# Performance work log

Hardware: AMD Instinct MI355X
Metric: run time of the kernel (lower is better)

Reference implementation:

```python
import jax, jax.numpy as jnp
import numpy as np
import math

COV_WEIGHT = 1.0
BANDWIDTH_FACTOR = 1.06
SQRT_2PI = math.sqrt(2.0 * math.pi)
EPS_LOG = 1e-8
H_MIN = 1e-4


def setup_inputs() -> dict:
    key = jax.random.key(0)
    activity = jax.random.normal(key, (2048, 64), dtype=jnp.float32)
    return {"activity": activity}


def reference(activity):
    B, R = activity.shape
    # Silverman bandwidth per receptor (torch .std uses ddof=1)
    std = jnp.std(activity, axis=0, ddof=1)                     # (R,)
    h = jnp.maximum(BANDWIDTH_FACTOR * std * (B ** (-0.2)), H_MIN)  # (R,)

    # Pairwise Gaussian KDE: query == samples == activity
    u = (activity[:, None, :] - activity[None, :, :]) / h       # (B_q, B_s, R)
    kernel_values = jnp.exp(-0.5 * u * u) / SQRT_2PI             # (B_q, B_s, R)
    density = kernel_values.sum(axis=1) / (B * h)                # (B_q, R)

    entropies = -jnp.mean(jnp.log(density + EPS_LOG), axis=0)    # (R,)
    loss_entropy = -entropies.mean()

    # Covariance penalty: sum of squared off-diagonals
    centered = activity - activity.mean(axis=0, keepdims=True)
    cov = (centered.T @ centered) / (B - 1)                      # (R, R)
    off = cov - jnp.diag(jnp.diag(cov))
    loss_cov = jnp.sum(off * off)

    total_loss = loss_entropy + COV_WEIGHT * loss_cov
    return total_loss
```

## Files before the change

### kernel.cpp

```cpp
#include <hip/hip_runtime.h>
#include <math.h>

#define B_SZ 2048
#define R_SZ 64
#define Q_TILE 4
#define SG_N 16

#define B_POW_NEG02 0.217637640824031f
#define SQRT_2PI 2.5066282746310002f
#define LOG2E 1.44269504088896340736f

extern "C" __device__ float __ocml_native_exp2_f32(float);

__global__ __launch_bounds__(1024) void cov_stats_kernel(const float* __restrict__ A,
                                                         float* __restrict__ kscale,
                                                         float* __restrict__ lscale,
                                                         float* __restrict__ cov_partial) {
    int i = blockIdx.x;
    int tid = threadIdx.x;
    int j = tid & 63, bg = tid >> 6;

    float g = 0.f, sj = 0.f;
#pragma unroll 4
    for (int b = bg; b < B_SZ; b += SG_N) {
        float ai = A[b * R_SZ + i];
        float aj = A[b * R_SZ + j];
        g = fmaf(ai, aj, g);
        sj += aj;
    }

    __shared__ float gred[SG_N][64];
    __shared__ float sred[SG_N][64];
    __shared__ float gfin[64], sfin[64];
    gred[bg][j] = g;
    sred[bg][j] = sj;
    __syncthreads();
    if (tid < 64) {
        float G = 0.f, S = 0.f;
#pragma unroll
        for (int t = 0; t < SG_N; ++t) { G += gred[t][j]; S += sred[t][j]; }
        gfin[j] = G;
        sfin[j] = S;
    }
    __syncthreads();
    if (tid < 64) {
        float m_j = sfin[j] * (1.f / (float)B_SZ);
        float m_i = sfin[i] * (1.f / (float)B_SZ);
        float cov = (gfin[j] - (float)B_SZ * m_i * m_j) * (1.f / (float)(B_SZ - 1));
        float v = (j == i) ? 0.f : cov * cov;
        for (int off = 32; off > 0; off >>= 1) v += __shfl_down(v, off, 64);
        if (j == 0) cov_partial[i] = v;
        if (j == i) {
            float var = (gfin[i] - sfin[i] * m_i) * (1.f / (float)(B_SZ - 1));
            var = fmaxf(var, 0.f);
            float h = fmaxf(1.06f * sqrtf(var) * B_POW_NEG02, 1e-4f);
            kscale[i] = sqrtf(0.5f * LOG2E) / h;
            lscale[i] = 1.0f / ((float)B_SZ * h * SQRT_2PI);
        }
    }
}

__global__ __launch_bounds__(1024) void kde_kernel(const float* __restrict__ A,
                                                   const float* __restrict__ kscale,
                                                   const float* __restrict__ lscale,
                                                   float* __restrict__ kde_partial) {
    int tid = threadIdx.x;
    int r = tid & 63, sg = tid >> 6;
    int q0 = blockIdx.x * Q_TILE;
    float k = kscale[r];
    float a0 = A[(q0 + 0) * R_SZ + r] * k;
    float a1 = A[(q0 + 1) * R_SZ + r] * k;
    float a2 = A[(q0 + 2) * R_SZ + r] * k;
    float a3 = A[(q0 + 3) * R_SZ + r] * k;
    float c0 = 0.f, c1 = 0.f, c2 = 0.f, c3 = 0.f;
#pragma unroll 4
    for (int s = sg; s < B_SZ; s += SG_N) {
        float as = A[s * R_SZ + r] * k;
        float d;
        d = a0 - as; c0 += __ocml_native_exp2_f32(-d * d);
        d = a1 - as; c1 += __ocml_native_exp2_f32(-d * d);
        d = a2 - as; c2 += __ocml_native_exp2_f32(-d * d);
        d = a3 - as; c3 += __ocml_native_exp2_f32(-d * d);
    }
    __shared__ float lds[SG_N][Q_TILE][64];
    lds[sg][0][r] = c0;
    lds[sg][1][r] = c1;
    lds[sg][2][r] = c2;
    lds[sg][3][r] = c3;
    __syncthreads();
    __shared__ float wred[Q_TILE];
    if (sg < Q_TILE) {
        float S = 0.f;
#pragma unroll
        for (int t = 0; t < SG_N; ++t) S += lds[t][sg][r];
        float v = __logf(fmaf(S, lscale[r], 1e-8f));
        for (int off = 32; off > 0; off >>= 1) v += __shfl_down(v, off, 64);
        if (r == 0) wred[sg] = v;
    }
    __syncthreads();
    if (tid == 0) {
        kde_partial[blockIdx.x] = (wred[0] + wred[1] + wred[2] + wred[3]) *
                                  (1.0f / ((float)B_SZ * (float)R_SZ));
    }
}

__global__ __launch_bounds__(256) void final_kernel(const float* __restrict__ partials,
                                                    int n, float* __restrict__ out) {
    int tid = threadIdx.x;
    float v = 0.f;
    for (int idx = tid; idx < n; idx += 256) v += partials[idx];
    for (int off = 32; off > 0; off >>= 1) v += __shfl_down(v, off, 64);
    __shared__ float wr[4];
    int wave = tid >> 6, lane = tid & 63;
    if (lane == 0) wr[wave] = v;
    __syncthreads();
    if (tid == 0) out[0] = wr[0] + wr[1] + wr[2] + wr[3];
}

extern "C" void kernel_launch(void* const* d_in, const int* in_sizes, int n_in,
                              void* d_out, int out_size, void* d_ws, size_t ws_size,
                              hipStream_t stream) {
    const float* A = (const float*)d_in[0];
    float* out = (float*)d_out;

    float* wsf = (float*)d_ws;
    float* kscale      = wsf;
    float* lscale      = wsf + 64;
    float* cov_partial = wsf + 128;
    float* kde_partial = wsf + 192;

    cov_stats_kernel<<<R_SZ, 1024, 0, stream>>>(A, kscale, lscale, cov_partial);
    kde_kernel<<<B_SZ / Q_TILE, 1024, 0, stream>>>(A, kscale, lscale, kde_partial);
    final_kernel<<<1, 256, 0, stream>>>(cov_partial, 64 + B_SZ / Q_TILE, out);
}
```

Baseline: 104.1 us.

## Exploit KDE kernel symmetry with triangular tile pairs and atomic density accumulation

Replaces the full pairwise KDE sweep with a symmetric tiling: only upper-triangular 64x64 tile pairs are evaluated, and each exp value is credited to both the query row and the sample row through LDS and global atomics. This roughly halves the exp work. In exchange it adds LDS atomics in the inner loop, global atomics into a zeroed density buffer, a memset, and a separate entropy kernel. The final reduction now reads 128 partials, covering the covariance and entropy partials laid out contiguously in the workspace.

```diff
diff --git a/kernel.cpp b/kernel.cpp
--- a/kernel.cpp
+++ b/kernel.cpp
@@ -3,14 +3,15 @@
 
 #define B_SZ 2048
 #define R_SZ 64
-#define Q_TILE 4
-#define SG_N 16
+#define TS 64
+#define NTILE 32
 
 #define B_POW_NEG02 0.217637640824031f
 #define SQRT_2PI 2.5066282746310002f
 #define LOG2E 1.44269504088896340736f
 
 extern "C" __device__ float __ocml_native_exp2_f32(float);
+
 
 __global__ __launch_bounds__(1024) void cov_stats_kernel(const float* __restrict__ A,
                                                          float* __restrict__ kscale,
@@ -22,15 +23,15 @@
 
     float g = 0.f, sj = 0.f;
 #pragma unroll 4
-    for (int b = bg; b < B_SZ; b += SG_N) {
+    for (int b = bg; b < B_SZ; b += 16) {
         float ai = A[b * R_SZ + i];
         float aj = A[b * R_SZ + j];
         g = fmaf(ai, aj, g);
         sj += aj;
     }
 
-    __shared__ float gred[SG_N][64];
-    __shared__ float sred[SG_N][64];
+    __shared__ float gred[16][64];
+    __shared__ float sred[16][64];
     __shared__ float gfin[64], sfin[64];
     gred[bg][j] = g;
     sred[bg][j] = sj;
@@ -38,7 +39,7 @@
     if (tid < 64) {
         float G = 0.f, S = 0.f;
 #pragma unroll
-        for (int t = 0; t < SG_N; ++t) { G += gred[t][j]; S += sred[t][j]; }
+        for (int t = 0; t < 16; ++t) { G += gred[t][j]; S += sred[t][j]; }
         gfin[j] = G;
         sfin[j] = S;
     }
@@ -60,61 +61,107 @@
     }
 }
 
-__global__ __launch_bounds__(1024) void kde_kernel(const float* __restrict__ A,
-                                                   const float* __restrict__ kscale,
-                                                   const float* __restrict__ lscale,
-                                                   float* __restrict__ kde_partial) {
+__global__ __launch_bounds__(1024) void kde_sym_kernel(const float* __restrict__ A,
+                                                       const float* __restrict__ kscale,
+                                                       float* __restrict__ density) {
+    __shared__ float Ls[TS][R_SZ];
+    __shared__ float colbuf[TS][R_SZ];
+
     int tid = threadIdx.x;
-    int r = tid & 63, sg = tid >> 6;
-    int q0 = blockIdx.x * Q_TILE;
+    int r = tid & 63, w = tid >> 6;
+
+    int t = blockIdx.x;
+    int ti, tj;
+    bool diag;
+    if (t < NTILE) {
+        ti = tj = t; diag = true;
+    } else {
+        int p = t - NTILE; diag = false;
+        ti = 0;
+        int cnt = NTILE - 1;
+        while (p >= cnt) { p -= cnt; ti++; cnt--; }
+        tj = ti + 1 + p;
+    }
+    int q0 = ti * TS, s0 = tj * TS;
+
     float k = kscale[r];
-    float a0 = A[(q0 + 0) * R_SZ + r] * k;
-    float a1 = A[(q0 + 1) * R_SZ + r] * k;
-    float a2 = A[(q0 + 2) * R_SZ + r] * k;
-    float a3 = A[(q0 + 3) * R_SZ + r] * k;
-    float c0 = 0.f, c1 = 0.f, c2 = 0.f, c3 = 0.f;
-#pragma unroll 4
-    for (int s = sg; s < B_SZ; s += SG_N) {
-        float as = A[s * R_SZ + r] * k;
-        float d;
-        d = a0 - as; c0 += __ocml_native_exp2_f32(-d * d);
-        d = a1 - as; c1 += __ocml_native_exp2_f32(-d * d);
-        d = a2 - as; c2 += __ocml_native_exp2_f32(-d * d);
-        d = a3 - as; c3 += __ocml_native_exp2_f32(-d * d);
+
+#pragma unroll
+    for (int i = 0; i < 4; ++i) {
+        int srow = w + 16 * i;
+        Ls[srow][r] = A[(s0 + srow) * R_SZ + r] * k;
+        colbuf[srow][r] = 0.f;
     }
-    __shared__ float lds[SG_N][Q_TILE][64];
-    lds[sg][0][r] = c0;
-    lds[sg][1][r] = c1;
-    lds[sg][2][r] = c2;
-    lds[sg][3][r] = c3;
+    float aq0 = A[(q0 + w +  0) * R_SZ + r] * k;
+    float aq1 = A[(q0 + w + 16) * R_SZ + r] * k;
+    float aq2 = A[(q0 + w + 32) * R_SZ + r] * k;
+    float aq3 = A[(q0 + w + 48) * R_SZ + r] * k;
     __syncthreads();
-    __shared__ float wred[Q_TILE];
-    if (sg < Q_TILE) {
-        float S = 0.f;
+
+    float r0 = 0.f, r1 = 0.f, r2 = 0.f, r3 = 0.f;
+    int sstart = 4 * w;
+#pragma unroll 1
+    for (int pass = 0; pass < 2; ++pass) {
+        int lo = (pass == 0) ? sstart : 0;
+        int hi = (pass == 0) ? TS : sstart;
+        for (int s = lo; s < hi; ++s) {
+            float as = Ls[s][r];
+            float d0 = aq0 - as, d1 = aq1 - as, d2 = aq2 - as, d3 = aq3 - as;
+            float e0 = __ocml_native_exp2_f32(-d0 * d0);
+            float e1 = __ocml_native_exp2_f32(-d1 * d1);
+            float e2 = __ocml_native_exp2_f32(-d2 * d2);
+            float e3 = __ocml_native_exp2_f32(-d3 * d3);
+            r0 += e0; r1 += e1; r2 += e2; r3 += e3;
+            if (!diag)
+                atomicAdd(&colbuf[s][r], (e0 + e1) + (e2 + e3));
+        }
+    }
+
+    atomicAdd(&density[(q0 + w +  0) * R_SZ + r], r0);
+    atomicAdd(&density[(q0 + w + 16) * R_SZ + r], r1);
+    atomicAdd(&density[(q0 + w + 32) * R_SZ + r], r2);
+    atomicAdd(&density[(q0 + w + 48) * R_SZ + r], r3);
+
+    if (!diag) {
+        __syncthreads();
 #pragma unroll
-        for (int t = 0; t < SG_N; ++t) S += lds[t][sg][r];
-        float v = __logf(fmaf(S, lscale[r], 1e-8f));
-        for (int off = 32; off > 0; off >>= 1) v += __shfl_down(v, off, 64);
-        if (r == 0) wred[sg] = v;
-    }
-    __syncthreads();
-    if (tid == 0) {
-        kde_partial[blockIdx.x] = (wred[0] + wred[1] + wred[2] + wred[3]) *
-                                  (1.0f / ((float)B_SZ * (float)R_SZ));
+        for (int i = 0; i < 4; ++i) {
+            int srow = w + 16 * i;
+            atomicAdd(&density[(s0 + srow) * R_SZ + r], colbuf[srow][r]);
+        }
     }
 }
 
-__global__ __launch_bounds__(256) void final_kernel(const float* __restrict__ partials,
-                                                    int n, float* __restrict__ out) {
+__global__ __launch_bounds__(1024) void entropy_kernel(const float* __restrict__ density,
+                                                       const float* __restrict__ lscale,
+                                                       float* __restrict__ ent_partial) {
     int tid = threadIdx.x;
-    float v = 0.f;
-    for (int idx = tid; idx < n; idx += 256) v += partials[idx];
+    int r = tid & 63;
+    float ls = lscale[r];
+    int base = blockIdx.x * 2048 + tid;
+    float v = __logf(fmaf(density[base], ls, 1e-8f))
+            + __logf(fmaf(density[base + 1024], ls, 1e-8f));
     for (int off = 32; off > 0; off >>= 1) v += __shfl_down(v, off, 64);
-    __shared__ float wr[4];
-    int wave = tid >> 6, lane = tid & 63;
-    if (lane == 0) wr[wave] = v;
+    __shared__ float wr[16];
+    if ((tid & 63) == 0) wr[tid >> 6] = v;
     __syncthreads();
-    if (tid == 0) out[0] = wr[0] + wr[1] + wr[2] + wr[3];
+    if (tid == 0) {
+        float s = 0.f;
+#pragma unroll
+        for (int i = 0; i < 16; ++i) s += wr[i];
+        ent_partial[blockIdx.x] = s * (1.0f / ((float)B_SZ * (float)R_SZ));
+    }
+}
+
+__global__ __launch_bounds__(128) void final_kernel(const float* __restrict__ partials,
+                                                    float* __restrict__ out) {
+    int tid = threadIdx.x;
+    float v = partials[tid];
+    for (int off = 32; off > 0; off >>= 1) v += __shfl_down(v, off, 64);
+    __shared__ float wr[2];
+    if ((tid & 63) == 0) wr[tid >> 6] = v;
+    __syncthreads();
+    if (tid == 0) out[0] = wr[0] + wr[1];
 }
 
 extern "C" void kernel_launch(void* const* d_in, const int* in_sizes, int n_in,
@@ -127,9 +174,12 @@
     float* kscale      = wsf;
     float* lscale      = wsf + 64;
     float* cov_partial = wsf + 128;
-    float* kde_partial = wsf + 192;
+    float* ent_partial = wsf + 192;
+    float* density     = wsf + 256;
 
+    hipMemsetAsync((void*)density, 0, B_SZ * R_SZ * sizeof(float), stream);
     cov_stats_kernel<<<R_SZ, 1024, 0, stream>>>(A, kscale, lscale, cov_partial);
-    kde_kernel<<<B_SZ / Q_TILE, 1024, 0, stream>>>(A, kscale, lscale, kde_partial);
-    final_kernel<<<1, 256, 0, stream>>>(cov_partial, 64 + B_SZ / Q_TILE, out);
+    kde_sym_kernel<<<NTILE + (NTILE * (NTILE - 1)) / 2, 1024, 0, stream>>>(A, kscale, density);
+    entropy_kernel<<<64, 1024, 0, stream>>>(density, lscale, ent_partial);
+    final_kernel<<<1, 128, 0, stream>>>(cov_partial, out);
 }
```

New measurement: 242.4 us. 2.33x slower.

## Prescale activity once, stage samples in LDS, fuse final reduction via last-block atomics

Applied to the files above, without the earlier changes.

The stats kernel now computes per-receptor variance in every block, writes a bandwidth-prescaled copy of the activity matrix to workspace, and resets the accumulators. The KDE kernel reads sample chunks of that prescaled matrix into shared memory with float4 copies instead of per-sample global loads with a multiply. The separate final kernel is removed: each block atomically adds its entropy partial and the last block sums the covariance partials and writes the output. This cuts one launch and the per-sample scaling, but adds atomics, a global write of the scaled matrix, and a barrier pair per chunk.

```diff
diff --git a/kernel.cpp b/kernel.cpp
--- a/kernel.cpp
+++ b/kernel.cpp
@@ -3,8 +3,10 @@
 
 #define B_SZ 2048
 #define R_SZ 64
-#define Q_TILE 4
-#define SG_N 16
+#define QT 4
+#define CH 128
+#define NCHUNK (B_SZ / CH)
+#define KDE_BLOCKS (B_SZ / QT)
 
 #define B_POW_NEG02 0.217637640824031f
 #define SQRT_2PI 2.5066282746310002f
@@ -12,35 +14,43 @@
 
 extern "C" __device__ float __ocml_native_exp2_f32(float);
 
+
 __global__ __launch_bounds__(1024) void cov_stats_kernel(const float* __restrict__ A,
-                                                         float* __restrict__ kscale,
+                                                         float* __restrict__ U,
                                                          float* __restrict__ lscale,
-                                                         float* __restrict__ cov_partial) {
+                                                         float* __restrict__ cov_partial,
+                                                         float* __restrict__ ent_acc,
+                                                         int* __restrict__ done_cnt) {
     int i = blockIdx.x;
     int tid = threadIdx.x;
     int j = tid & 63, bg = tid >> 6;
 
-    float g = 0.f, sj = 0.f;
+    float g = 0.f, sj = 0.f, s2j = 0.f;
 #pragma unroll 4
-    for (int b = bg; b < B_SZ; b += SG_N) {
+    for (int b = bg; b < B_SZ; b += 16) {
         float ai = A[b * R_SZ + i];
         float aj = A[b * R_SZ + j];
         g = fmaf(ai, aj, g);
         sj += aj;
+        s2j = fmaf(aj, aj, s2j);
     }
 
-    __shared__ float gred[SG_N][64];
-    __shared__ float sred[SG_N][64];
-    __shared__ float gfin[64], sfin[64];
-    gred[bg][j] = g;
-    sred[bg][j] = sj;
+    __shared__ float gred[16][64], sred[16][64], s2red[16][64];
+    __shared__ float gfin[64], sfin[64], hs[64];
+    gred[bg][j] = g; sred[bg][j] = sj; s2red[bg][j] = s2j;
     __syncthreads();
     if (tid < 64) {
-        float G = 0.f, S = 0.f;
+        float G = 0.f, S = 0.f, S2 = 0.f;
 #pragma unroll
-        for (int t = 0; t < SG_N; ++t) { G += gred[t][j]; S += sred[t][j]; }
+        for (int t = 0; t < 16; ++t) { G += gred[t][j]; S += sred[t][j]; S2 += s2red[t][j]; }
         gfin[j] = G;
         sfin[j] = S;
+        float m = S * (1.f / (float)B_SZ);
+        float var = (S2 - S * m) * (1.f / (float)(B_SZ - 1));
+        var = fmaxf(var, 0.f);
+        float h = fmaxf(1.06f * sqrtf(var) * B_POW_NEG02, 1e-4f);
+        hs[j] = sqrtf(0.5f * LOG2E) / h;
+        if (i == 0) lscale[j] = 1.0f / ((float)B_SZ * h * SQRT_2PI);
     }
     __syncthreads();
     if (tid < 64) {
@@ -50,71 +60,85 @@
         float v = (j == i) ? 0.f : cov * cov;
         for (int off = 32; off > 0; off >>= 1) v += __shfl_down(v, off, 64);
         if (j == 0) cov_partial[i] = v;
-        if (j == i) {
-            float var = (gfin[i] - sfin[i] * m_i) * (1.f / (float)(B_SZ - 1));
-            var = fmaxf(var, 0.f);
-            float h = fmaxf(1.06f * sqrtf(var) * B_POW_NEG02, 1e-4f);
-            kscale[i] = sqrtf(0.5f * LOG2E) / h;
-            lscale[i] = 1.0f / ((float)B_SZ * h * SQRT_2PI);
-        }
     }
+    if (i == 0 && tid == 64) { *ent_acc = 0.f; *done_cnt = 0; }
+
+    int base = i * (32 * R_SZ);
+    float k0 = hs[tid & 63];
+    U[base + tid]        = A[base + tid]        * k0;
+    U[base + 1024 + tid] = A[base + 1024 + tid] * k0;
 }
 
-__global__ __launch_bounds__(1024) void kde_kernel(const float* __restrict__ A,
-                                                   const float* __restrict__ kscale,
+__global__ __launch_bounds__(1024) void kde_kernel(const float* __restrict__ U,
                                                    const float* __restrict__ lscale,
-                                                   float* __restrict__ kde_partial) {
+                                                   const float* __restrict__ cov_partial,
+                                                   float* __restrict__ ent_acc,
+                                                   int* __restrict__ done_cnt,
+                                                   float* __restrict__ out) {
+    __shared__ float Us[CH * R_SZ];
     int tid = threadIdx.x;
     int r = tid & 63, sg = tid >> 6;
-    int q0 = blockIdx.x * Q_TILE;
-    float k = kscale[r];
-    float a0 = A[(q0 + 0) * R_SZ + r] * k;
-    float a1 = A[(q0 + 1) * R_SZ + r] * k;
-    float a2 = A[(q0 + 2) * R_SZ + r] * k;
-    float a3 = A[(q0 + 3) * R_SZ + r] * k;
+    int q0 = blockIdx.x * QT;
+
+    float uq0 = U[(q0 + 0) * R_SZ + r];
+    float uq1 = U[(q0 + 1) * R_SZ + r];
+    float uq2 = U[(q0 + 2) * R_SZ + r];
+    float uq3 = U[(q0 + 3) * R_SZ + r];
     float c0 = 0.f, c1 = 0.f, c2 = 0.f, c3 = 0.f;
-#pragma unroll 4
-    for (int s = sg; s < B_SZ; s += SG_N) {
-        float as = A[s * R_SZ + r] * k;
-        float d;
-        d = a0 - as; c0 += __ocml_native_exp2_f32(-d * d);
-        d = a1 - as; c1 += __ocml_native_exp2_f32(-d * d);
-        d = a2 - as; c2 += __ocml_native_exp2_f32(-d * d);
-        d = a3 - as; c3 += __ocml_native_exp2_f32(-d * d);
+
+    for (int ch = 0; ch < NCHUNK; ++ch) {
+        const float4* src = (const float4*)(U + ch * (CH * R_SZ));
+        float4* dst = (float4*)Us;
+        dst[tid]        = src[tid];
+        dst[tid + 1024] = src[tid + 1024];
+        __syncthreads();
+#pragma unroll
+        for (int it = 0; it < CH / 16; ++it) {
+            float us = Us[(sg + 16 * it) * R_SZ + r];
+            float d0 = uq0 - us; c0 += __ocml_native_exp2_f32(-d0 * d0);
+            float d1 = uq1 - us; c1 += __ocml_native_exp2_f32(-d1 * d1);
+            float d2 = uq2 - us; c2 += __ocml_native_exp2_f32(-d2 * d2);
+            float d3 = uq3 - us; c3 += __ocml_native_exp2_f32(-d3 * d3);
+        }
+        __syncthreads();
     }
-    __shared__ float lds[SG_N][Q_TILE][64];
-    lds[sg][0][r] = c0;
-    lds[sg][1][r] = c1;
-    lds[sg][2][r] = c2;
-    lds[sg][3][r] = c3;
+
+    float (*red)[QT][64] = (float (*)[QT][64])Us;
+    red[sg][0][r] = c0;
+    red[sg][1][r] = c1;
+    red[sg][2][r] = c2;
+    red[sg][3][r] = c3;
     __syncthreads();
-    __shared__ float wred[Q_TILE];
-    if (sg < Q_TILE) {
+    __shared__ float wred[QT];
+    if (sg < QT) {
         float S = 0.f;
 #pragma unroll
-        for (int t = 0; t < SG_N; ++t) S += lds[t][sg][r];
+        for (int t = 0; t < 16; ++t) S += red[t][sg][r];
         float v = __logf(fmaf(S, lscale[r], 1e-8f));
         for (int off = 32; off > 0; off >>= 1) v += __shfl_down(v, off, 64);
         if (r == 0) wred[sg] = v;
     }
     __syncthreads();
+    __shared__ int lastflag;
     if (tid == 0) {
-        kde_partial[blockIdx.x] = (wred[0] + wred[1] + wred[2] + wred[3]) *
-                                  (1.0f / ((float)B_SZ * (float)R_SZ));
+        float p = (wred[0] + wred[1] + wred[2] + wred[3]) *
+                  (1.0f / ((float)B_SZ * (float)R_SZ));
+        atomicAdd(ent_acc, p);
+        __threadfence();
+        int prev = atomicAdd(done_cnt, 1);
+        lastflag = (prev == KDE_BLOCKS - 1);
     }
-}
-
-__global__ __launch_bounds__(256) void final_kernel(const float* __restrict__ partials,
-                                                    int n, float* __restrict__ out) {
-    int tid = threadIdx.x;
-    float v = 0.f;
-    for (int idx = tid; idx < n; idx += 256) v += partials[idx];
-    for (int off = 32; off > 0; off >>= 1) v += __shfl_down(v, off, 64);
-    __shared__ float wr[4];
-    int wave = tid >> 6, lane = tid & 63;
-    if (lane == 0) wr[wave] = v;
     __syncthreads();
-    if (tid == 0) out[0] = wr[0] + wr[1] + wr[2] + wr[3];
+    if (lastflag && tid < 64) {
+        __threadfence();
+        float v = cov_partial[tid];
+        for (int off = 32; off > 0; off >>= 1) v += __shfl_down(v, off, 64);
+        if (tid == 0) {
+            float ent = __hip_atomic_load(ent_acc, __ATOMIC_ACQUIRE,
+                                          __HIP_MEMORY_SCOPE_AGENT);
+            out[0] = ent + v;
+        }
+    }
 }
 
 extern "C" void kernel_launch(void* const* d_in, const int* in_sizes, int n_in,
@@ -124,12 +148,14 @@
     float* out = (float*)d_out;
 
     float* wsf = (float*)d_ws;
-    float* kscale      = wsf;
-    float* lscale      = wsf + 64;
-    float* cov_partial = wsf + 128;
-    float* kde_partial = wsf + 192;
+    float* lscale      = wsf;
+    float* cov_partial = wsf + 64;
+    float* ent_acc     = wsf + 160;
+    int*   done_cnt    = (int*)(wsf + 192);
+    float* U           = wsf + 256;
 
-    cov_stats_kernel<<<R_SZ, 1024, 0, stream>>>(A, kscale, lscale, cov_partial);
-    kde_kernel<<<B_SZ / Q_TILE, 1024, 0, stream>>>(A, kscale, lscale, kde_partial);
-    final_kernel<<<1, 256, 0, stream>>>(cov_partial, 64 + B_SZ / Q_TILE, out);
+    cov_stats_kernel<<<R_SZ, 1024, 0, stream>>>(A, U, lscale, cov_partial,
+                                                ent_acc, done_cnt);
+    kde_kernel<<<KDE_BLOCKS, 1024, 0, stream>>>(U, lscale, cov_partial,
+                                                ent_acc, done_cnt, out);
 }
```

Result: slower. 108.6 us (+4.4%).
